# Kernel tuning notes

Hardware: AMD Instinct MI355X
Metric: run time of the kernel (lower is better)

Reference implementation:

```python
import jax, jax.numpy as jnp
import numpy as np

N_HEADS = 8

def setup_inputs() -> dict:
    key = jax.random.key(0)
    qkv = jax.random.normal(key, (4, 1, 3 * N_HEADS * 64, 2048), dtype=jnp.float32)
    return {"qkv": qkv}

def reference(qkv):
    # qkv: [N, G, 3*H*C, T]
    bs, groups, width, length = qkv.shape
    ch = width // (3 * N_HEADS)
    q, k, v = jnp.split(qkv, 3, axis=2)
    scale = 1.0 / np.sqrt(ch)  # applied to BOTH q and k (as in original)
    qr = (q * scale).reshape(bs, groups, N_HEADS, ch, length)
    kr = (k * scale).reshape(bs, groups, N_HEADS, ch, length)
    vr = v.reshape(bs, groups, N_HEADS, ch, length)
    weight = jnp.einsum('bghct,bghcs->bghts', qr, kr)  # [N,G,H,T,T]
    weight = jax.nn.softmax(weight.astype(jnp.float32), axis=-1).astype(qkv.dtype)
    a = jnp.einsum('bghts,bghcs->bghct', weight, vr)  # [N,G,H,C,T]
    return a.reshape(bs, -1, length)  # [N, G*H*C, T]
```

## Files before the change

kernel.cpp:

```cpp
#include <hip/hip_runtime.h>
#include <hip/hip_bf16.h>

typedef __attribute__((ext_vector_type(4))) float f32x4;
typedef __attribute__((ext_vector_type(16))) float f32x16;
typedef __attribute__((ext_vector_type(4))) float f4;
typedef __attribute__((ext_vector_type(8))) short bf16x8;
typedef __attribute__((ext_vector_type(4))) short s16x4;
typedef __attribute__((ext_vector_type(4))) unsigned u32x4;

#define T_LEN 2048
#define SPAD 72
#define QSCALE 0.022542110013890054f

#define SWZ(r) (((r) ^ ((r) >> 3)) & 7)

__device__ inline short f2bf(float f) {
  unsigned u = __builtin_bit_cast(unsigned, f);
  return (short)((u + 0x7fffu + ((u >> 16) & 1u)) >> 16);
}

__global__ __launch_bounds__(256) void prep_t(const float* __restrict__ qkv,
                                              short* __restrict__ qt,
                                              short* __restrict__ kt) {
  __shared__ float tile[64][65];
  const int bid = blockIdx.x;
  const int tch = bid & 31;
  const int head = (bid >> 5) & 31;
  const int sel = bid >> 10;
  const int b = head >> 3, h = head & 7;
  const float* src = qkv + ((size_t)b * 1536 + sel * 512 + h * 64) * T_LEN + tch * 64;
  short* dst = (sel ? kt : qt) + (size_t)head * T_LEN * 64 + (size_t)tch * 64 * 64;
  const int tid = threadIdx.x;
  const float sc = sel ? 1.0f : QSCALE;

  for (int e = tid; e < 4096; e += 256) {
    int c = e >> 6, t = e & 63;
    tile[c][t] = src[(size_t)c * T_LEN + t];
  }
  __syncthreads();
  for (int e = tid; e < 2048; e += 256) {
    int t = e >> 5, c2 = (e & 31) * 2;
    unsigned lo = (unsigned short)f2bf(tile[c2][t] * sc);
    unsigned hi = (unsigned short)f2bf(tile[c2 + 1][t] * sc);
    int cdst = sel ? (c2 ^ (SWZ(t) << 3)) : c2;
    *(unsigned*)&dst[t * 64 + cdst] = lo | (hi << 16);
  }
}

__global__ __launch_bounds__(256) void prep_v(const float* __restrict__ qkv,
                                              short* __restrict__ v_out) {
  int id = blockIdx.x * 256 + threadIdx.x;
  int s4 = id & 15;
  int c = (id >> 4) & 63;
  int stile = (id >> 10) & 31;
  int head = id >> 15;
  int b = head >> 3, h = head & 7;
  const float* src =
      qkv + ((size_t)b * 1536 + 1024 + h * 64 + c) * T_LEN + stile * 64 + s4 * 4;
  f4 s = *(const f4*)src;
  s16x4 o;
#pragma unroll
  for (int j = 0; j < 4; ++j) o[j] = f2bf(s[j]);
  size_t dsts = (((size_t)head * 32 + stile) * 64 + c) * 64 + ((s4 * 4) ^ (SWZ(c) << 3));
  *(s16x4*)&v_out[dsts] = o;
}

__global__ __launch_bounds__(512, 4) void attn13(const short* __restrict__ Qt,
                                                 const short* __restrict__ Kt,
                                                 const short* __restrict__ Vb,
                                                 float* __restrict__ out) {
  __shared__ short KV[2][2][2][4096];

  const int bid = blockIdx.x;
  const int head = bid & 31;
  const int qblk = bid >> 5;

  const int tid = threadIdx.x;
  const int wave = tid >> 6;
  const int grp = wave >> 2;
  const int wv = wave & 3;
  const int lane = tid & 63;
  const int l31 = lane & 31;
  const int hi = lane >> 5;

  const int t0 = qblk * 128 + wv * 32;
  const int sbase = grp * 16;

  const short* Qh = Qt + (size_t)head * 131072;
  const short* Kh = Kt + (size_t)head * 131072;
  const short* Vh = Vb + (size_t)head * 131072;
  float* O = out + (size_t)head * 131072;

  const int sw0 = SWZ(l31) << 3;
  const int sw1 = SWZ(l31 + 32) << 3;

  auto stage = [&](int buf, int it) {
#pragma unroll
    for (int j = 0; j < 4; ++j) {
      const int chunk = wv * 4 + j;
      const short* g =
          (chunk < 8 ? Kh : Vh) + (sbase + it) * 4096 + (chunk & 7) * 512 + lane * 8;
      short* l = &KV[grp][buf][chunk >> 3][(chunk & 7) * 512];
      __builtin_amdgcn_global_load_lds((const __attribute__((address_space(1))) void*)g,
                                       (__attribute__((address_space(3))) void*)l,
                                       16, 0, 0);
    }
  };

  bf16x8 aq[4];
#pragma unroll
  for (int ck = 0; ck < 4; ++ck)
    aq[ck] = *(const bf16x8*)&Qh[(size_t)(t0 + l31) * 64 + ck * 16 + hi * 8];

  float l_lane = 0.f;
  f32x16 o_acc[2];
#pragma unroll
  for (int j = 0; j < 16; ++j) { o_acc[0][j] = 0.f; o_acc[1][j] = 0.f; }

  auto tile_body = [&](int buf) {
    f32x16 s0, s1;
#pragma unroll
    for (int j = 0; j < 16; ++j) { s0[j] = 0.f; s1[j] = 0.f; }
    __builtin_amdgcn_s_setprio(1);
#pragma unroll
    for (int ck = 0; ck < 4; ++ck) {
      const bf16x8 k0 = *(const bf16x8*)&KV[grp][buf][0][l31 * 64 + ((ck * 16 + hi * 8) ^ sw0)];
      s0 = __builtin_amdgcn_mfma_f32_32x32x16_bf16(k0, aq[ck], s0, 0, 0, 0);
      const bf16x8 k1 = *(const bf16x8*)&KV[grp][buf][0][(32 + l31) * 64 + ((ck * 16 + hi * 8) ^ sw1)];
      s1 = __builtin_amdgcn_mfma_f32_32x32x16_bf16(k1, aq[ck], s1, 0, 0, 0);
    }
    __builtin_amdgcn_s_setprio(0);

    float ps0 = 0.f, ps1 = 0.f, ps2 = 0.f, ps3 = 0.f;
    bf16x8 pf[4];
    const f32x16* sv[2] = {&s0, &s1};
#pragma unroll
    for (int sbk = 0; sbk < 2; ++sbk) {
      float p[16];
#pragma unroll
      for (int j = 0; j < 16; ++j) p[j] = __builtin_amdgcn_exp2f((*sv[sbk])[j]);
      ps0 += p[0] + p[4] + p[8] + p[12];
      ps1 += p[1] + p[5] + p[9] + p[13];
      ps2 += p[2] + p[6] + p[10] + p[14];
      ps3 += p[3] + p[7] + p[11] + p[15];
      unsigned w0, w1, w2, w3, w4, w5, w6, w7;
      asm("v_cvt_pk_bf16_f32 %0, %1, %2" : "=v"(w0) : "v"(p[0]), "v"(p[1]));
      asm("v_cvt_pk_bf16_f32 %0, %1, %2" : "=v"(w1) : "v"(p[2]), "v"(p[3]));
      asm("v_cvt_pk_bf16_f32 %0, %1, %2" : "=v"(w2) : "v"(p[4]), "v"(p[5]));
      asm("v_cvt_pk_bf16_f32 %0, %1, %2" : "=v"(w3) : "v"(p[6]), "v"(p[7]));
      asm("v_cvt_pk_bf16_f32 %0, %1, %2" : "=v"(w4) : "v"(p[8]), "v"(p[9]));
      asm("v_cvt_pk_bf16_f32 %0, %1, %2" : "=v"(w5) : "v"(p[10]), "v"(p[11]));
      asm("v_cvt_pk_bf16_f32 %0, %1, %2" : "=v"(w6) : "v"(p[12]), "v"(p[13]));
      asm("v_cvt_pk_bf16_f32 %0, %1, %2" : "=v"(w7) : "v"(p[14]), "v"(p[15]));
      asm("v_permlane32_swap_b32 %0, %1" : "+v"(w0), "+v"(w2));
      asm("v_permlane32_swap_b32 %0, %1" : "+v"(w1), "+v"(w3));
      asm("v_permlane32_swap_b32 %0, %1" : "+v"(w4), "+v"(w6));
      asm("v_permlane32_swap_b32 %0, %1" : "+v"(w5), "+v"(w7));
      u32x4 fe = {w0, w1, w2, w3};
      u32x4 fo = {w4, w5, w6, w7};
      pf[sbk * 2] = __builtin_bit_cast(bf16x8, fe);
      pf[sbk * 2 + 1] = __builtin_bit_cast(bf16x8, fo);
    }
    l_lane += (ps0 + ps1) + (ps2 + ps3);

    __builtin_amdgcn_s_setprio(1);
#pragma unroll
    for (int sc = 0; sc < 4; ++sc) {
      const bf16x8 v0 = *(const bf16x8*)&KV[grp][buf][1][l31 * 64 + ((sc * 16 + hi * 8) ^ sw0)];
      o_acc[0] = __builtin_amdgcn_mfma_f32_32x32x16_bf16(v0, pf[sc], o_acc[0], 0, 0, 0);
      const bf16x8 v1 = *(const bf16x8*)&KV[grp][buf][1][(32 + l31) * 64 + ((sc * 16 + hi * 8) ^ sw1)];
      o_acc[1] = __builtin_amdgcn_mfma_f32_32x32x16_bf16(v1, pf[sc], o_acc[1], 0, 0, 0);
    }
    __builtin_amdgcn_s_setprio(0);
  };

  stage(0, 0);
  __syncthreads();

  for (int itp = 0; itp < 8; ++itp) {
    const int it = itp * 2;
    stage(1, it + 1);
    tile_body(0);
    __syncthreads();
    if (itp < 7) stage(0, it + 2);
    tile_body(1);
    __syncthreads();
  }

  const float lg = l_lane + __shfl_xor(l_lane, 32, 64);
  float* xb = (float*)&KV[0][0][0][0];
  if (grp == 1) {
    float* dst = xb + (wv * 64 + lane) * 33;
#pragma unroll
    for (int j = 0; j < 16; ++j) { dst[j] = o_acc[0][j]; dst[16 + j] = o_acc[1][j]; }
    dst[32] = lg;
  }
  __syncthreads();
  if (grp == 0) {
    const float* src = xb + (wv * 64 + lane) * 33;
    const float rl = 1.0f / (lg + src[32]);
#pragma unroll
    for (int j = 0; j < 16; ++j) {
      const int c0 = (j & 3) + 8 * (j >> 2) + 4 * hi;
      O[(size_t)c0 * T_LEN + t0 + l31] = (o_acc[0][j] + src[j]) * rl;
      O[(size_t)(32 + c0) * T_LEN + t0 + l31] = (o_acc[1][j] + src[16 + j]) * rl;
    }
  }
}

__global__ __launch_bounds__(256) void attn_fwd(const float* __restrict__ qkv,
                                                float* __restrict__ out) {
  __shared__ short KtS[64][SPAD];
  __shared__ short VtS[64][SPAD];
  __shared__ short PbS[4][16][SPAD];

  const int bid = blockIdx.x;
  const int qt = bid & 31;
  const int head = bid >> 5;
  const int b = head >> 3, h = head & 7;

  const size_t base = ((size_t)b * 1536 + h * 64) * T_LEN;
  const float* Q = qkv + base;
  const float* K = qkv + base + (size_t)512 * T_LEN;
  const float* V = qkv + base + (size_t)1024 * T_LEN;
  float* O = out + ((size_t)b * 512 + h * 64) * T_LEN;

  const int tid = threadIdx.x;
  const int wave = tid >> 6;
  const int lane = tid & 63;
  const int l15 = lane & 15;
  const int l4 = lane >> 4;
  const int t0 = qt * 64 + wave * 16;

  bf16x8 aq[2];
#pragma unroll
  for (int kk = 0; kk < 2; ++kk)
#pragma unroll
    for (int j = 0; j < 8; ++j) {
      int c = kk * 32 + l4 * 8 + j;
      aq[kk][j] = f2bf(Q[(size_t)c * T_LEN + t0 + l15]);
    }

  float m_run[4], l_run[4];
  f32x4 o_acc[4];
#pragma unroll
  for (int r = 0; r < 4; ++r) { m_run[r] = -1e30f; l_run[r] = 0.f; }
#pragma unroll
  for (int n = 0; n < 4; ++n) o_acc[n] = (f32x4){0.f, 0.f, 0.f, 0.f};

  const float inv64 = 0.015625f;

  for (int s0 = 0; s0 < T_LEN; s0 += 64) {
    __syncthreads();
    for (int e = tid; e < 4096; e += 256) {
      int c = e >> 6, s = e & 63;
      KtS[s][c] = f2bf(K[(size_t)c * T_LEN + s0 + s]);
      VtS[c][s] = f2bf(V[(size_t)c * T_LEN + s0 + s]);
    }
    __syncthreads();

    f32x4 sacc[4];
#pragma unroll
    for (int n = 0; n < 4; ++n) {
      const bf16x8 bk0 = *(const bf16x8*)&KtS[16 * n + l15][l4 * 8];
      const bf16x8 bk1 = *(const bf16x8*)&KtS[16 * n + l15][32 + l4 * 8];
      f32x4 z = (f32x4){0.f, 0.f, 0.f, 0.f};
      z = __builtin_amdgcn_mfma_f32_16x16x32_bf16(aq[0], bk0, z, 0, 0, 0);
      z = __builtin_amdgcn_mfma_f32_16x16x32_bf16(aq[1], bk1, z, 0, 0, 0);
      sacc[n] = z;
    }

#pragma unroll
    for (int r = 0; r < 4; ++r) {
      float mx = fmaxf(fmaxf(sacc[0][r], sacc[1][r]),
                       fmaxf(sacc[2][r], sacc[3][r])) * inv64;
#pragma unroll
      for (int off = 8; off >= 1; off >>= 1)
        mx = fmaxf(mx, __shfl_xor(mx, off, 64));
      const float m_new = fmaxf(m_run[r], mx);
      const float alpha = __expf(m_run[r] - m_new);
      float psum = 0.f;
#pragma unroll
      for (int n = 0; n < 4; ++n) {
        float p = __expf(sacc[n][r] * inv64 - m_new);
        psum += p;
        PbS[wave][l4 * 4 + r][16 * n + l15] = f2bf(p);
      }
#pragma unroll
      for (int off = 8; off >= 1; off >>= 1)
        psum += __shfl_xor(psum, off, 64);
      l_run[r] = l_run[r] * alpha + psum;
      m_run[r] = m_new;
#pragma unroll
      for (int n = 0; n < 4; ++n) o_acc[n][r] *= alpha;
    }

    const bf16x8 ap0 = *(const bf16x8*)&PbS[wave][l15][l4 * 8];
    const bf16x8 ap1 = *(const bf16x8*)&PbS[wave][l15][32 + l4 * 8];
#pragma unroll
    for (int n = 0; n < 4; ++n) {
      const bf16x8 bv0 = *(const bf16x8*)&VtS[16 * n + l15][l4 * 8];
      const bf16x8 bv1 = *(const bf16x8*)&VtS[16 * n + l15][32 + l4 * 8];
      o_acc[n] = __builtin_amdgcn_mfma_f32_16x16x32_bf16(ap0, bv0, o_acc[n], 0, 0, 0);
      o_acc[n] = __builtin_amdgcn_mfma_f32_16x16x32_bf16(ap1, bv1, o_acc[n], 0, 0, 0);
    }
  }

#pragma unroll
  for (int n = 0; n < 4; ++n)
#pragma unroll
    for (int r = 0; r < 4; ++r) {
      const int c = 16 * n + l15;
      const int t = t0 + l4 * 4 + r;
      O[(size_t)c * T_LEN + t] = o_acc[n][r] / l_run[r];
    }
}

extern "C" void kernel_launch(void* const* d_in, const int* in_sizes, int n_in,
                              void* d_out, int out_size, void* d_ws, size_t ws_size,
                              hipStream_t stream) {
  const float* qkv = (const float*)d_in[0];
  float* out = (float*)d_out;
  const size_t per_buf = (size_t)32 * T_LEN * 64;
  const size_t need = per_buf * 3 * sizeof(short);
  if (ws_size >= need) {
    short* qt = (short*)d_ws;
    short* kt = qt + per_buf;
    short* vb = kt + per_buf;
    hipLaunchKernelGGL(prep_t, dim3(2048), dim3(256), 0, stream, qkv, qt, kt);
    hipLaunchKernelGGL(prep_v, dim3(4096), dim3(256), 0, stream, qkv, vb);
    hipLaunchKernelGGL(attn13, dim3(512), dim3(512), 0, stream, qt, kt, vb, out);
  } else {
    hipLaunchKernelGGL(attn_fwd, dim3(1024), dim3(256), 0, stream, qkv, out);
  }
}
```

Before: 58.40 us.

## Merge K/V prep kernels, load Q directly in attention, sum rowsums via MFMA

Combines the K-transpose and V-convert prep kernels into one launch. Q preprocessing is dropped, and the attention kernel reads Q straight from fp32 qkv, scaling it and converting to bf16 in registers. Softmax row sums now come from an extra MFMA against a ones vector instead of VALU adds and a cross-lane shuffle. This removes one launch, one workspace buffer and some VALU work, at the cost of uncoalesced strided fp32 Q loads and extra MFMA issue in the inner loop.

```diff
diff --git a/kernel.cpp b/kernel.cpp
--- a/kernel.cpp
+++ b/kernel.cpp
@@ -19,53 +19,52 @@
   return (short)((u + 0x7fffu + ((u >> 16) & 1u)) >> 16);
 }
 
-__global__ __launch_bounds__(256) void prep_t(const float* __restrict__ qkv,
-                                              short* __restrict__ qt,
-                                              short* __restrict__ kt) {
+__global__ __launch_bounds__(256) void prep(const float* __restrict__ qkv,
+                                            short* __restrict__ kt,
+                                            short* __restrict__ vb) {
   __shared__ float tile[64][65];
   const int bid = blockIdx.x;
-  const int tch = bid & 31;
-  const int head = (bid >> 5) & 31;
-  const int sel = bid >> 10;
-  const int b = head >> 3, h = head & 7;
-  const float* src = qkv + ((size_t)b * 1536 + sel * 512 + h * 64) * T_LEN + tch * 64;
-  short* dst = (sel ? kt : qt) + (size_t)head * T_LEN * 64 + (size_t)tch * 64 * 64;
   const int tid = threadIdx.x;
-  const float sc = sel ? 1.0f : QSCALE;
-
-  for (int e = tid; e < 4096; e += 256) {
-    int c = e >> 6, t = e & 63;
-    tile[c][t] = src[(size_t)c * T_LEN + t];
-  }
-  __syncthreads();
-  for (int e = tid; e < 2048; e += 256) {
-    int t = e >> 5, c2 = (e & 31) * 2;
-    unsigned lo = (unsigned short)f2bf(tile[c2][t] * sc);
-    unsigned hi = (unsigned short)f2bf(tile[c2 + 1][t] * sc);
-    int cdst = sel ? (c2 ^ (SWZ(t) << 3)) : c2;
-    *(unsigned*)&dst[t * 64 + cdst] = lo | (hi << 16);
-  }
-}
-
-__global__ __launch_bounds__(256) void prep_v(const float* __restrict__ qkv,
-                                              short* __restrict__ v_out) {
-  int id = blockIdx.x * 256 + threadIdx.x;
-  int s4 = id & 15;
-  int c = (id >> 4) & 63;
-  int stile = (id >> 10) & 31;
-  int head = id >> 15;
-  int b = head >> 3, h = head & 7;
-  const float* src =
-      qkv + ((size_t)b * 1536 + 1024 + h * 64 + c) * T_LEN + stile * 64 + s4 * 4;
-  f4 s = *(const f4*)src;
-  s16x4 o;
-#pragma unroll
-  for (int j = 0; j < 4; ++j) o[j] = f2bf(s[j]);
-  size_t dsts = (((size_t)head * 32 + stile) * 64 + c) * 64 + ((s4 * 4) ^ (SWZ(c) << 3));
-  *(s16x4*)&v_out[dsts] = o;
-}
-
-__global__ __launch_bounds__(512, 4) void attn13(const short* __restrict__ Qt,
+
+  if (bid < 1024) {
+    const int tch = bid & 31;
+    const int head = bid >> 5;
+    const int b = head >> 3, h = head & 7;
+    const float* src = qkv + ((size_t)b * 1536 + 512 + h * 64) * T_LEN + tch * 64;
+    short* dst = kt + (size_t)head * 131072 + (size_t)tch * 4096;
+
+    for (int e = tid; e < 4096; e += 256) {
+      int c = e >> 6, t = e & 63;
+      tile[c][t] = src[(size_t)c * T_LEN + t];
+    }
+    __syncthreads();
+    for (int e = tid; e < 2048; e += 256) {
+      int t = e >> 5, c2 = (e & 31) * 2;
+      unsigned lo = (unsigned short)f2bf(tile[c2][t]);
+      unsigned hi = (unsigned short)f2bf(tile[c2 + 1][t]);
+      int cdst = c2 ^ (SWZ(t) << 3);
+      *(unsigned*)&dst[t * 64 + cdst] = lo | (hi << 16);
+    }
+  } else {
+    int id = (bid - 1024) * 256 + tid;
+    int s4 = id & 15;
+    int c = (id >> 4) & 63;
+    int stile = (id >> 10) & 31;
+    int head = id >> 15;
+    int b = head >> 3, h = head & 7;
+    const float* src =
+        qkv + ((size_t)b * 1536 + 1024 + h * 64 + c) * T_LEN + stile * 64 + s4 * 4;
+    f4 s = *(const f4*)src;
+    s16x4 o;
+#pragma unroll
+    for (int j = 0; j < 4; ++j) o[j] = f2bf(s[j]);
+    size_t dsts =
+        (((size_t)head * 32 + stile) * 64 + c) * 64 + ((s4 * 4) ^ (SWZ(c) << 3));
+    *(s16x4*)&vb[dsts] = o;
+  }
+}
+
+__global__ __launch_bounds__(512, 4) void attn14(const float* __restrict__ qkv,
                                                  const short* __restrict__ Kt,
                                                  const short* __restrict__ Vb,
                                                  float* __restrict__ out) {
@@ -86,7 +85,8 @@
   const int t0 = qblk * 128 + wv * 32;
   const int sbase = grp * 16;
 
-  const short* Qh = Qt + (size_t)head * 131072;
+  const int b = head >> 3, h = head & 7;
+  const float* Qf = qkv + ((size_t)b * 1536 + h * 64) * T_LEN;
   const short* Kh = Kt + (size_t)head * 131072;
   const short* Vh = Vb + (size_t)head * 131072;
   float* O = out + (size_t)head * 131072;
@@ -107,15 +107,27 @@
     }
   };
 
+  stage(0, 0);
+
   bf16x8 aq[4];
 #pragma unroll
-  for (int ck = 0; ck < 4; ++ck)
-    aq[ck] = *(const bf16x8*)&Qh[(size_t)(t0 + l31) * 64 + ck * 16 + hi * 8];
-
-  float l_lane = 0.f;
+  for (int ck = 0; ck < 4; ++ck) {
+    float qv[8];
+#pragma unroll
+    for (int j = 0; j < 8; ++j)
+      qv[j] = Qf[(size_t)(ck * 16 + hi * 8 + j) * T_LEN + t0 + l31];
+#pragma unroll
+    for (int j = 0; j < 8; ++j) aq[ck][j] = f2bf(qv[j] * QSCALE);
+  }
+
+  bf16x8 ones;
+#pragma unroll
+  for (int j = 0; j < 8; ++j) ones[j] = (short)0x3F80;
+
+  f32x16 l_acc;
   f32x16 o_acc[2];
 #pragma unroll
-  for (int j = 0; j < 16; ++j) { o_acc[0][j] = 0.f; o_acc[1][j] = 0.f; }
+  for (int j = 0; j < 16; ++j) { o_acc[0][j] = 0.f; o_acc[1][j] = 0.f; l_acc[j] = 0.f; }
 
   auto tile_body = [&](int buf) {
     f32x16 s0, s1;
@@ -131,7 +143,6 @@
     }
     __builtin_amdgcn_s_setprio(0);
 
-    float ps0 = 0.f, ps1 = 0.f, ps2 = 0.f, ps3 = 0.f;
     bf16x8 pf[4];
     const f32x16* sv[2] = {&s0, &s1};
 #pragma unroll
@@ -139,10 +150,6 @@
       float p[16];
 #pragma unroll
       for (int j = 0; j < 16; ++j) p[j] = __builtin_amdgcn_exp2f((*sv[sbk])[j]);
-      ps0 += p[0] + p[4] + p[8] + p[12];
-      ps1 += p[1] + p[5] + p[9] + p[13];
-      ps2 += p[2] + p[6] + p[10] + p[14];
-      ps3 += p[3] + p[7] + p[11] + p[15];
       unsigned w0, w1, w2, w3, w4, w5, w6, w7;
       asm("v_cvt_pk_bf16_f32 %0, %1, %2" : "=v"(w0) : "v"(p[0]), "v"(p[1]));
       asm("v_cvt_pk_bf16_f32 %0, %1, %2" : "=v"(w1) : "v"(p[2]), "v"(p[3]));
@@ -161,7 +168,6 @@
       pf[sbk * 2] = __builtin_bit_cast(bf16x8, fe);
       pf[sbk * 2 + 1] = __builtin_bit_cast(bf16x8, fo);
     }
-    l_lane += (ps0 + ps1) + (ps2 + ps3);
 
     __builtin_amdgcn_s_setprio(1);
 #pragma unroll
@@ -170,11 +176,11 @@
       o_acc[0] = __builtin_amdgcn_mfma_f32_32x32x16_bf16(v0, pf[sc], o_acc[0], 0, 0, 0);
       const bf16x8 v1 = *(const bf16x8*)&KV[grp][buf][1][(32 + l31) * 64 + ((sc * 16 + hi * 8) ^ sw1)];
       o_acc[1] = __builtin_amdgcn_mfma_f32_32x32x16_bf16(v1, pf[sc], o_acc[1], 0, 0, 0);
+      l_acc = __builtin_amdgcn_mfma_f32_32x32x16_bf16(ones, pf[sc], l_acc, 0, 0, 0);
     }
     __builtin_amdgcn_s_setprio(0);
   };
 
-  stage(0, 0);
   __syncthreads();
 
   for (int itp = 0; itp < 8; ++itp) {
@@ -187,7 +193,7 @@
     __syncthreads();
   }
 
-  const float lg = l_lane + __shfl_xor(l_lane, 32, 64);
+  const float lg = l_acc[0];
   float* xb = (float*)&KV[0][0][0][0];
   if (grp == 1) {
     float* dst = xb + (wv * 64 + lane) * 33;
@@ -322,14 +328,12 @@
   const float* qkv = (const float*)d_in[0];
   float* out = (float*)d_out;
   const size_t per_buf = (size_t)32 * T_LEN * 64;
-  const size_t need = per_buf * 3 * sizeof(short);
+  const size_t need = per_buf * 2 * sizeof(short);
   if (ws_size >= need) {
-    short* qt = (short*)d_ws;
-    short* kt = qt + per_buf;
+    short* kt = (short*)d_ws;
     short* vb = kt + per_buf;
-    hipLaunchKernelGGL(prep_t, dim3(2048), dim3(256), 0, stream, qkv, qt, kt);
-    hipLaunchKernelGGL(prep_v, dim3(4096), dim3(256), 0, stream, qkv, vb);
-    hipLaunchKernelGGL(attn13, dim3(512), dim3(512), 0, stream, qt, kt, vb, out);
+    hipLaunchKernelGGL(prep, dim3(5120), dim3(256), 0, stream, qkv, kt, vb);
+    hipLaunchKernelGGL(attn14, dim3(512), dim3(512), 0, stream, qkv, kt, vb, out);
   } else {
     hipLaunchKernelGGL(attn_fwd, dim3(1024), dim3(256), 0, stream, qkv, out);
   }
```

After: 55.03 us. 1.06x faster.
